# Kernel tuning notes

Measured on AMD Instinct MI355X. Metric: run time of the kernel, lower is better.

## Reference

```python
import jax, jax.numpy as jnp
import numpy as np

WS = 14          # window size
NH = 12          # num heads
C = 768          # hidden dim
HD = C // NH     # head dim = 64
MLP = 3072       # mlp dim
EPS = 1e-6


def _layernorm(x, g, b):
    mu = jnp.mean(x, axis=-1, keepdims=True)
    var = jnp.mean(jnp.square(x - mu), axis=-1, keepdims=True)
    return (x - mu) * jax.lax.rsqrt(var + EPS) * g + b


def setup_inputs() -> dict:
    key = jax.random.key(0)
    ks = jax.random.split(key, 8)
    B, H, W = 8, 64, 64
    f32 = jnp.float32
    d = {}
    d["x"] = jax.random.normal(ks[0], (B, H, W, C), f32)
    d["ln1_g"] = jnp.ones((C,), f32)
    d["ln1_b"] = jnp.zeros((C,), f32)
    d["qkv_w"] = (jax.random.normal(ks[1], (C, 3 * C), f32) * 0.02)
    d["qkv_b"] = jnp.zeros((3 * C,), f32)
    d["proj_w"] = (jax.random.normal(ks[2], (C, C), f32) * 0.02)
    d["proj_b"] = jnp.zeros((C,), f32)
    d["rel_pos_h"] = (jax.random.normal(ks[3], (2 * WS - 1, HD), f32) * 0.02)
    d["rel_pos_w"] = (jax.random.normal(ks[4], (2 * WS - 1, HD), f32) * 0.02)
    d["ln2_g"] = jnp.ones((C,), f32)
    d["ln2_b"] = jnp.zeros((C,), f32)
    d["mlp_w1"] = (jax.random.normal(ks[5], (C, MLP), f32) * 0.02)
    d["mlp_b1"] = jnp.zeros((MLP,), f32)
    d["mlp_w2"] = (jax.random.normal(ks[6], (MLP, C), f32) * 0.02)
    d["mlp_b2"] = jnp.zeros((C,), f32)
    return d


def reference(x, ln1_g, ln1_b, qkv_w, qkv_b, proj_w, proj_b,
              rel_pos_h, rel_pos_w, ln2_g, ln2_b,
              mlp_w1, mlp_b1, mlp_w2, mlp_b2):
    B, H, W, _ = x.shape
    xn = _layernorm(x, ln1_g, ln1_b)

    # ---- window partition (pad to multiple of WS) ----
    pad_h = (-H) % WS
    pad_w = (-W) % WS
    Hp, Wp = H + pad_h, W + pad_w
    xp = jnp.pad(xn, ((0, 0), (0, pad_h), (0, pad_w), (0, 0)))
    # [B, Hp/WS, WS, Wp/WS, WS, C] -> [Bn, WS, WS, C]
    win = xp.reshape(B, Hp // WS, WS, Wp // WS, WS, C)
    win = win.transpose(0, 1, 3, 2, 4, 5).reshape(-1, WS, WS, C)
    Bn = win.shape[0]
    N = WS * WS

    # ---- attention with decomposed relative position bias ----
    qkv = win.reshape(Bn, N, C) @ qkv_w + qkv_b                 # [Bn, N, 3C]
    qkv = qkv.reshape(Bn, N, 3, NH, HD).transpose(2, 0, 3, 1, 4)
    qkv = qkv.reshape(3, Bn * NH, N, HD)
    q, k, v = qkv[0], qkv[1], qkv[2]

    scale = HD ** -0.5
    attn = jnp.einsum('bnd,bmd->bnm', q * scale, k)             # [Bn*NH, N, N]

    # rel coords: q_size == k_size == WS, rel_pos already has 2*WS-1 rows
    coords = jnp.arange(WS)[:, None] - jnp.arange(WS)[None, :] + (WS - 1)
    Rh = rel_pos_h[coords]                                      # [WS, WS, HD]
    Rw = rel_pos_w[coords]                                      # [WS, WS, HD]
    rq = q.reshape(Bn * NH, WS, WS, HD)
    rel_h = jnp.einsum('bhwc,hkc->bhwk', rq, Rh)                # [B', WS, WS, WS]
    rel_w = jnp.einsum('bhwc,wkc->bhwk', rq, Rw)
    attn = (attn.reshape(Bn * NH, WS, WS, WS, WS)
            + rel_h[:, :, :, :, None]
            + rel_w[:, :, :, None, :]).reshape(Bn * NH, N, N)

    attn = jax.nn.softmax(attn, axis=-1)
    out = jnp.einsum('bnm,bmd->bnd', attn, v)                   # [Bn*NH, N, HD]
    out = out.reshape(Bn, NH, WS, WS, HD).transpose(0, 2, 3, 1, 4).reshape(Bn, WS, WS, C)
    out = out @ proj_w + proj_b

    # ---- window unpartition ----
    out = out.reshape(B, Hp // WS, Wp // WS, WS, WS, C)
    out = out.transpose(0, 1, 3, 2, 4, 5).reshape(B, Hp, Wp, C)[:, :H, :W, :]

    x1 = x + out
    y = _layernorm(x1, ln2_g, ln2_b)
    y = jax.nn.gelu(y @ mlp_w1 + mlp_b1, approximate=False) @ mlp_w2 + mlp_b2
    return x1 + y
```

## Files before the change

kernel.cpp:

```cpp
#include <hip/hip_runtime.h>
#include <hip/hip_bf16.h>
#include <cstdint>
#include <cstddef>

using bf16 = __hip_bfloat16;
typedef __attribute__((ext_vector_type(8))) short short8;
typedef __attribute__((ext_vector_type(4))) float f32x4;

typedef __attribute__((address_space(1))) const void as1_void;
typedef __attribute__((address_space(3))) void as3_void;

__device__ __forceinline__ f32x4 mfma16x16x32(short8 a, short8 b, f32x4 c) {
  return __builtin_amdgcn_mfma_f32_16x16x32_bf16(a, b, c, 0, 0, 0);
}

__device__ __forceinline__ void gload_lds16(const void* g, void* l) {
  __builtin_amdgcn_global_load_lds((as1_void*)g, (as3_void*)l, 16, 0, 0);
}

__device__ __forceinline__ uint32_t cvtpk(float a, float b) {
  uint32_t r;
  asm("v_cvt_pk_bf16_f32 %0, %1, %2" : "=v"(r) : "v"(a), "v"(b));
  return r;
}


static constexpr int MROWS = 39200;
static constexpr int MPAD  = 39296;
static constexpr int TOK2  = 32768;

__global__ __launch_bounds__(256)
void transpose_cast(const float* __restrict__ in, bf16* __restrict__ out, int K, int N) {
  __shared__ float t[32][33];
  const int tx = threadIdx.x & 31, ty = threadIdx.x >> 5;
  const int bx = blockIdx.x, by = blockIdx.y;
  const int x = bx * 32 + tx;
  for (int r = ty; r < 32; r += 8)
    t[r][tx] = in[(size_t)(by * 32 + r) * N + x];
  __syncthreads();
  const int xo = by * 32 + tx;
  for (int r = ty; r < 32; r += 8)
    out[(size_t)(bx * 32 + r) * K + xo] = __float2bfloat16(t[tx][r]);
}

__global__ __launch_bounds__(256)
void ln1_partition(const float* __restrict__ x, const float* __restrict__ g,
                   const float* __restrict__ bb, bf16* __restrict__ out) {
  const int token = blockIdx.x * 4 + (threadIdx.x >> 6);
  const int lane = threadIdx.x & 63;
  const int win = token / 196, tok = token % 196;
  const int b_ = win / 25, wh = (win / 5) % 5, ww = win % 5;
  const int i = tok / 14, j = tok % 14;
  const int h = wh * 14 + i, w = ww * 14 + j;
  bf16* o = out + (size_t)token * 768;
  if (h >= 64 || w >= 64) {
    for (int t = 0; t < 12; ++t) o[lane + 64 * t] = __float2bfloat16(0.f);
    return;
  }
  const float* src = x + ((size_t)((b_ * 64 + h) * 64 + w)) * 768;
  float vals[12], s = 0.f, ss = 0.f;
  #pragma unroll
  for (int t = 0; t < 12; ++t) {
    float v = src[lane + 64 * t];
    vals[t] = v; s += v; ss += v * v;
  }
  #pragma unroll
  for (int d = 32; d > 0; d >>= 1) { s += __shfl_xor(s, d); ss += __shfl_xor(ss, d); }
  const float mu = s * (1.f / 768.f);
  const float var = ss * (1.f / 768.f) - mu * mu;
  const float inv = rsqrtf(var + 1e-6f);
  #pragma unroll
  for (int t = 0; t < 12; ++t) {
    const int c = lane + 64 * t;
    o[c] = __float2bfloat16((vals[t] - mu) * inv * g[c] + bb[c]);
  }
}

__global__ __launch_bounds__(256)
void ln2_kernel(const float* __restrict__ x1, const float* __restrict__ g,
                const float* __restrict__ bb, bf16* __restrict__ out) {
  const int token = blockIdx.x * 4 + (threadIdx.x >> 6);
  const int lane = threadIdx.x & 63;
  const float* src = x1 + (size_t)token * 768;
  bf16* o = out + (size_t)token * 768;
  float vals[12], s = 0.f, ss = 0.f;
  #pragma unroll
  for (int t = 0; t < 12; ++t) {
    float v = src[lane + 64 * t];
    vals[t] = v; s += v; ss += v * v;
  }
  #pragma unroll
  for (int d = 32; d > 0; d >>= 1) { s += __shfl_xor(s, d); ss += __shfl_xor(ss, d); }
  const float mu = s * (1.f / 768.f);
  const float var = ss * (1.f / 768.f) - mu * mu;
  const float inv = rsqrtf(var + 1e-6f);
  #pragma unroll
  for (int t = 0; t < 12; ++t) {
    const int c = lane + 64 * t;
    o[c] = __float2bfloat16((vals[t] - mu) * inv * g[c] + bb[c]);
  }
}

template<int EPI>
__global__ __launch_bounds__(256)
void gemm_bf16(const bf16* __restrict__ A, const bf16* __restrict__ Bt,
               const float* __restrict__ bias, int K, int Mreal,
               const float* __restrict__ fin, float* __restrict__ fout,
               bf16* __restrict__ ob0, bf16* __restrict__ ob1, bf16* __restrict__ ob2) {
  __shared__ __align__(16) bf16 SMEM[16384];
  bf16* const lA[2] = { SMEM, SMEM + 4096 };
  bf16* const lB[2] = { SMEM + 8192, SMEM + 12288 };
  const int tid = threadIdx.x;
  const int lane = tid & 63, wv = tid >> 6;
  const int lr = lane & 15, hi = lane >> 4;
  const int wm = wv >> 1, wn = wv & 1;

  const int gx = gridDim.x;
  const int nwg = gx * gridDim.y;
  int lin = blockIdx.y * gx + blockIdx.x;
  {
    const int q8 = nwg >> 3, r8 = nwg & 7;
    const int xcd = lin & 7, pos = lin >> 3;
    lin = (xcd < r8 ? xcd * (q8 + 1) : r8 * (q8 + 1) + (xcd - r8) * q8) + pos;
  }
  const size_t arow0 = (size_t)(lin / gx) * 128;
  const size_t brow0 = (size_t)(lin % gx) * 128;
  f32x4 acc[4][4] = {};

  auto stage = [&](bf16* bufA, bf16* bufB, int kt) {
    const int k0 = kt * 32;
    #pragma unroll
    for (int it = 0; it < 2; ++it) {
      const int seg = it * 256 + tid;
      const int row = seg >> 2, kq = seg & 3;
      const size_t dst = (size_t)(it * 256 + wv * 64) * 8;
      if constexpr (EPI == 1) {
        const int k = k0 + kq * 8;
        gload_lds16(A + ((size_t)(k >> 6) * MPAD + arow0 + row) * 64 + (k & 63), bufA + dst);
      } else {
        gload_lds16(A + (arow0 + row) * K + k0 + kq * 8, bufA + dst);
      }
      gload_lds16(Bt + (brow0 + row) * K + k0 + kq * 8, bufB + dst);
    }
  };
  auto compute = [&](const bf16* bufA, const bf16* bufB) {
    short8 af[4], bfr[4];
    #pragma unroll
    for (int m = 0; m < 4; ++m) af[m] = *(const short8*)&bufA[(wm * 64 + m * 16 + lr) * 32 + hi * 8];
    #pragma unroll
    for (int n = 0; n < 4; ++n) bfr[n] = *(const short8*)&bufB[(wn * 64 + n * 16 + lr) * 32 + hi * 8];
    #pragma unroll
    for (int m = 0; m < 4; ++m)
      #pragma unroll
      for (int n = 0; n < 4; ++n)
        acc[m][n] = mfma16x16x32(af[m], bfr[n], acc[m][n]);
  };

  const int nt = K >> 5;
  stage(lA[0], lB[0], 0);
  __syncthreads();
  for (int t = 0; t < nt; t += 2) {
    if (t + 1 < nt) stage(lA[1], lB[1], t + 1);
    compute(lA[0], lB[0]);
    __syncthreads();
    if (t + 2 < nt) stage(lA[0], lB[0], t + 2);
    compute(lA[1], lB[1]);
    __syncthreads();
  }

  if constexpr (EPI == 0 || EPI == 2) {
    bf16* ct = SMEM;
    #pragma unroll
    for (int n = 0; n < 4; ++n) {
      const int col = wn * 64 + n * 16 + lr;
      const float bv = bias[(int)brow0 + col];
      #pragma unroll
      for (int m = 0; m < 4; ++m) {
        #pragma unroll
        for (int e = 0; e < 4; ++e) {
          const int row = wm * 64 + m * 16 + hi * 4 + e;
          float v = acc[m][n][e] + bv;
          if constexpr (EPI == 2) v = 0.5f * v * (1.f + erff(v * 0.70710678118f));
          const int byte = (row << 8) + (col << 1);
          *(bf16*)((char*)ct + (byte ^ ((row & 7) << 5))) = __float2bfloat16(v);
        }
      }
    }
    __syncthreads();
    #pragma unroll
    for (int i = 0; i < 8; ++i) {
      const int lin16 = i * 256 + tid;
      const int row = lin16 >> 4;
      const int u   = lin16 & 15;
      const int byte = (row << 8) + (u << 4);
      const short8 val = *(const short8*)((char*)ct + (byte ^ ((row & 7) << 5)));
      const int grow = (int)arow0 + row;
      const int gcol = (int)brow0 + u * 8;
      if constexpr (EPI == 0) {
        if (grow < Mreal) {
          const int which = gcol / 768, head = (gcol >> 6) % 12, d = gcol & 63;
          bf16* dstb = (which == 0) ? ob0 : ((which == 1) ? ob1 : ob2);
          *(short8*)&dstb[((size_t)head * MPAD + grow) * 64 + d] = val;
        }
      } else {
        *(short8*)&ob0[(size_t)grow * 3072 + gcol] = val;
      }
    }
  } else {
    #pragma unroll
    for (int n = 0; n < 4; ++n) {
      const int col = (int)brow0 + wn * 64 + n * 16 + lr;
      const float bv = bias[col];
      #pragma unroll
      for (int m = 0; m < 4; ++m) {
        #pragma unroll
        for (int e = 0; e < 4; ++e) {
          const int row = (int)arow0 + wm * 64 + m * 16 + hi * 4 + e;
          const float v = acc[m][n][e] + bv;
          if constexpr (EPI == 1) {
            if (row < Mreal) {
              const int win = row / 196, tok = row % 196;
              const int b_ = win / 25, wh = (win / 5) % 5, ww = win % 5;
              const int i = tok / 14, j = tok % 14;
              const int h = wh * 14 + i, w = ww * 14 + j;
              if (h < 64 && w < 64) {
                const size_t idx = ((size_t)((b_ * 64 + h) * 64 + w)) * 768 + col;
                fout[idx] = fin[idx] + v;
              }
            }
          } else {
            const size_t idx = (size_t)row * 768 + col;
            fout[idx] = fin[idx] + v;
          }
        }
      }
    }
  }
}

__global__ __launch_bounds__(256)
void attn_kernel(const bf16* __restrict__ qb, const bf16* __restrict__ kb,
                 const bf16* __restrict__ vb, const float* __restrict__ rph,
                 const float* __restrict__ rpw, bf16* __restrict__ aout) {
  __shared__ __align__(16) char SM[65248];
  bf16* pbh    = (bf16*)SM;
  bf16* pbw    = (bf16*)(SM + 4096);
  bf16* Gh     = (bf16*)(SM + 8192);
  bf16* Gw     = (bf16*)(SM + 23168);
  char* klds   = SM;
  char* vtb    = SM + 25600;
  bf16* relh_s = (bf16*)(SM + 54272);
  bf16* relw_s = (bf16*)(SM + 59760);

  const int bh = blockIdx.x;
  const int win = bh / 12, head = bh % 12;
  const size_t base = ((size_t)head * MPAD + win * 196) * 64;
  const bf16* Q  = qb + base;
  const bf16* Kp = kb + base;
  const bf16* Vp = vb + base;
  const int tid = threadIdx.x, lane = tid & 63, wv = tid >> 6;
  const int lr = lane & 15, hi = lane >> 4;

  for (int i = tid; i < 32 * 64; i += 256) {
    const int r = i >> 6, c = i & 63;
    const bool ok = r < 27;
    pbh[i] = __float2bfloat16(ok ? rph[r * 64 + c] : 0.f);
    pbw[i] = __float2bfloat16(ok ? rpw[r * 64 + c] : 0.f);
  }
  __syncthreads();
  {
    short8 bh00 = *(const short8*)&pbh[(lr) * 64 + hi * 8];
    short8 bh01 = *(const short8*)&pbh[(lr) * 64 + 32 + hi * 8];
    short8 bh10 = *(const short8*)&pbh[(16 + lr) * 64 + hi * 8];
    short8 bh11 = *(const short8*)&pbh[(16 + lr) * 64 + 32 + hi * 8];
    short8 bw00 = *(const short8*)&pbw[(lr) * 64 + hi * 8];
    short8 bw01 = *(const short8*)&pbw[(lr) * 64 + 32 + hi * 8];
    short8 bw10 = *(const short8*)&pbw[(16 + lr) * 64 + hi * 8];
    short8 bw11 = *(const short8*)&pbw[(16 + lr) * 64 + 32 + hi * 8];
    for (int mt = wv; mt < 13; mt += 4) {
      const short8 a0 = *(const short8*)&Q[(mt * 16 + lr) * 64 + hi * 8];
      const short8 a1 = *(const short8*)&Q[(mt * 16 + lr) * 64 + 32 + hi * 8];
      f32x4 g0 = {}, g1 = {}, g2 = {}, g3 = {};
      g0 = mfma16x16x32(a0, bh00, g0); g0 = mfma16x16x32(a1, bh01, g0);
      g1 = mfma16x16x32(a0, bh10, g1); g1 = mfma16x16x32(a1, bh11, g1);
      g2 = mfma16x16x32(a0, bw00, g2); g2 = mfma16x16x32(a1, bw01, g2);
      g3 = mfma16x16x32(a0, bw10, g3); g3 = mfma16x16x32(a1, bw11, g3);
      #pragma unroll
      for (int e = 0; e < 4; ++e) {
        const int row = mt * 16 + hi * 4 + e;
        Gh[row * 36 + lr]      = __float2bfloat16(g0[e]);
        Gh[row * 36 + 16 + lr] = __float2bfloat16(g1[e]);
        Gw[row * 36 + lr]      = __float2bfloat16(g2[e]);
        Gw[row * 36 + 16 + lr] = __float2bfloat16(g3[e]);
      }
    }
  }
  __syncthreads();
  bf16 ghr[11], gwr[11];
  #pragma unroll
  for (int t = 0; t < 11; ++t) {
    const int i = tid + t * 256;
    if (i < 196 * 14) {
      const int q = i / 14, kk = i - (i / 14) * 14;
      const int rh = q / 14 - kk + 13;
      const int rw2 = q - (q / 14) * 14 - kk + 13;
      ghr[t] = Gh[q * 36 + rh];
      gwr[t] = Gw[q * 36 + rw2];
    }
  }
  __syncthreads();
  #pragma unroll
  for (int t = 0; t < 11; ++t) {
    const int i = tid + t * 256;
    if (i < 196 * 14) { relh_s[i] = ghr[t]; relw_s[i] = gwr[t]; }
  }
  for (int c = wv; c < 25; c += 4) {
    const int row = c * 8 + (lane >> 3);
    const int ch  = (lane & 7) ^ (row & 7);
    gload_lds16(Kp + row * 64 + ch * 8, klds + c * 1024);
  }
  for (int i = tid; i < 196 * 8; i += 256) {
    const int key = i >> 3, dg = (i & 7) * 8;
    const short8 v = *(const short8*)&Vp[key * 64 + dg];
    #pragma unroll
    for (int j = 0; j < 8; ++j) {
      const int idx = (dg + j) * 448 + key * 2;
      *(bf16*)(vtb + (idx ^ (j << 4))) = ((const bf16*)&v)[j];
    }
  }
  for (int i = tid; i < 64 * 28; i += 256) {
    const int d = i / 28, key = 196 + i - (i / 28) * 28;
    const int idx = d * 448 + key * 2;
    *(bf16*)(vtb + (idx ^ ((d & 7) << 4))) = __float2bfloat16(0.f);
  }
  __syncthreads();

  for (int qt = wv; qt < 13; qt += 4) {
    const int q = qt * 16 + lr;
    const int qc = q < 196 ? q : 195;
    const short8 bq0 = *(const short8*)&Q[(qt * 16 + lr) * 64 + hi * 8];
    const short8 bq1 = *(const short8*)&Q[(qt * 16 + lr) * 64 + 32 + hi * 8];
    f32x4 s[13];
    __builtin_amdgcn_s_setprio(1);
    #pragma unroll
    for (int nt = 0; nt < 13; ++nt) {
      const int key = nt * 16 + lr;
      const char* kr = klds + key * 128;
      const short8 ka0 = *(const short8*)(kr + (((hi) ^ (key & 7)) << 4));
      const short8 ka1 = *(const short8*)(kr + (((hi + 4) ^ (key & 7)) << 4));
      f32x4 z = {};
      z = mfma16x16x32(ka0, bq0, z);
      z = mfma16x16x32(ka1, bq1, z);
      s[nt] = z;
    }
    __builtin_amdgcn_s_setprio(0);
    float mx = -3.0e38f;
    #pragma unroll
    for (int nt = 0; nt < 13; ++nt) {
      #pragma unroll
      for (int e = 0; e < 4; ++e) {
        const int key = nt * 16 + hi * 4 + e;
        const int kh = key / 14, kw = key - kh * 14;
        float v = s[nt][e] * 0.125f + __bfloat162float(relh_s[qc * 14 + kh])
                                    + __bfloat162float(relw_s[qc * 14 + kw]);
        v = (key < 196) ? v : -3.0e38f;
        s[nt][e] = v;
        mx = fmaxf(mx, v);
      }
    }
    mx = fmaxf(mx, __shfl_xor(mx, 16));
    mx = fmaxf(mx, __shfl_xor(mx, 32));
    float sm = 0.f;
    #pragma unroll
    for (int nt = 0; nt < 13; ++nt)
      #pragma unroll
      for (int e = 0; e < 4; ++e) {
        const float p = __expf(s[nt][e] - mx);
        s[nt][e] = p; sm += p;
      }
    sm += __shfl_xor(sm, 16);
    sm += __shfl_xor(sm, 32);
    const float rinv = 1.f / sm;
    f32x4 o[4] = {};
    #pragma unroll
    for (int kk = 0; kk < 7; ++kk) {
      const uint32_t x0 = cvtpk(s[2 * kk][0] * rinv, s[2 * kk][1] * rinv);
      const uint32_t x1 = cvtpk(s[2 * kk][2] * rinv, s[2 * kk][3] * rinv);
      const uint32_t y0 = cvtpk(s[2 * kk + 1][0] * rinv, s[2 * kk + 1][1] * rinv);
      const uint32_t y1 = cvtpk(s[2 * kk + 1][2] * rinv, s[2 * kk + 1][3] * rinv);
      const uint32_t s0 = (hi < 2) ? y0 : x0, s1 = (hi < 2) ? y1 : x1;
      const uint32_t t0 = __shfl_xor(s0, 32), t1 = __shfl_xor(s1, 32);
      const uint32_t o0 = (hi < 2) ? x0 : y0, o1 = (hi < 2) ? x1 : y1;
      const bool sendOwn = (hi == 1) || (hi == 2);
      const uint32_t u0 = sendOwn ? o0 : t0, u1 = sendOwn ? o1 : t1;
      const uint32_t r0 = __shfl_xor(u0, 16), r1 = __shfl_xor(u1, 16);
      union { uint32_t u[4]; short8 v; } pf;
      pf.u[0] = (hi == 0) ? x0 : ((hi == 2) ? t0 : r0);
      pf.u[1] = (hi == 0) ? x1 : ((hi == 2) ? t1 : r1);
      pf.u[2] = (hi == 3) ? y0 : ((hi == 1) ? t0 : r0);
      pf.u[3] = (hi == 3) ? y1 : ((hi == 1) ? t1 : r1);
      __builtin_amdgcn_s_setprio(1);
      #pragma unroll
      for (int n2 = 0; n2 < 4; ++n2) {
        const int d = n2 * 16 + lr;
        const int idx = d * 448 + (kk * 32 + hi * 8) * 2;
        const short8 va = *(const short8*)(vtb + (idx ^ ((lr & 7) << 4)));
        o[n2] = mfma16x16x32(va, pf.v, o[n2]);
      }
      __builtin_amdgcn_s_setprio(0);
    }
    if (q < 196) {
      bf16* orow = aout + ((size_t)head * MPAD + win * 196 + q) * 64;
      #pragma unroll
      for (int n2 = 0; n2 < 4; ++n2) {
        uint32_t d0 = cvtpk(o[n2][0], o[n2][1]);
        uint32_t d1 = cvtpk(o[n2][2], o[n2][3]);
        uint32_t* dst = (uint32_t*)&orow[n2 * 16 + hi * 4];
        dst[0] = d0; dst[1] = d1;
      }
    }
  }
}

extern "C" void kernel_launch(void* const* d_in, const int* in_sizes, int n_in,
                              void* d_out, int out_size, void* d_ws, size_t ws_size,
                              hipStream_t stream) {
  (void)in_sizes; (void)n_in; (void)out_size; (void)ws_size;
  const float* x      = (const float*)d_in[0];
  const float* ln1_g  = (const float*)d_in[1];
  const float* ln1_b  = (const float*)d_in[2];
  const float* qkv_w  = (const float*)d_in[3];
  const float* qkv_b  = (const float*)d_in[4];
  const float* proj_w = (const float*)d_in[5];
  const float* proj_b = (const float*)d_in[6];
  const float* rph    = (const float*)d_in[7];
  const float* rpw    = (const float*)d_in[8];
  const float* ln2_g  = (const float*)d_in[9];
  const float* ln2_b  = (const float*)d_in[10];
  const float* w1     = (const float*)d_in[11];
  const float* b1v    = (const float*)d_in[12];
  const float* w2     = (const float*)d_in[13];
  const float* b2v    = (const float*)d_in[14];
  float* outp = (float*)d_out;

  char* ws = (char*)d_ws;
  size_t off = 0;
  auto alloc = [&](size_t bytes) { char* p = ws + off; off += (bytes + 255) & ~(size_t)255; return p; };
  bf16* qkv_wt  = (bf16*)alloc((size_t)2304 * 768 * 2);
  bf16* proj_wt = (bf16*)alloc((size_t)768 * 768 * 2);
  bf16* w1t     = (bf16*)alloc((size_t)3072 * 768 * 2);
  bf16* w2t     = (bf16*)alloc((size_t)768 * 3072 * 2);
  const size_t szB1 = (size_t)MPAD * 768 * 2;
  const size_t szB2 = (size_t)TOK2 * 768 * 2;
  char* regB = alloc(szB1 > szB2 ? szB1 : szB2);
  const size_t szQKV = (size_t)3 * 12 * MPAD * 64 * 2;
  const size_t szH   = (size_t)TOK2 * 3072 * 2;
  char* regC = alloc(szQKV > szH ? szQKV : szH);

  bf16* xnwin   = (bf16*)regB;
  bf16* attnout = (bf16*)regB;
  bf16* xn2     = (bf16*)regB;
  bf16* qbuf    = (bf16*)regC;
  bf16* kbuf    = qbuf + (size_t)12 * MPAD * 64;
  bf16* vbuf    = kbuf + (size_t)12 * MPAD * 64;
  bf16* hbuf    = (bf16*)regC;

  transpose_cast<<<dim3(2304 / 32, 768 / 32), 256, 0, stream>>>(qkv_w, qkv_wt, 768, 2304);
  transpose_cast<<<dim3(768 / 32, 768 / 32), 256, 0, stream>>>(proj_w, proj_wt, 768, 768);
  transpose_cast<<<dim3(3072 / 32, 768 / 32), 256, 0, stream>>>(w1, w1t, 768, 3072);
  transpose_cast<<<dim3(768 / 32, 3072 / 32), 256, 0, stream>>>(w2, w2t, 3072, 768);

  ln1_partition<<<dim3(MROWS / 4), 256, 0, stream>>>(x, ln1_g, ln1_b, xnwin);

  gemm_bf16<0><<<dim3(2304 / 128, MPAD / 128), 256, 0, stream>>>(
      xnwin, qkv_wt, qkv_b, 768, MROWS, nullptr, nullptr, qbuf, kbuf, vbuf);

  attn_kernel<<<dim3(2400), 256, 0, stream>>>(qbuf, kbuf, vbuf, rph, rpw, attnout);

  gemm_bf16<1><<<dim3(768 / 128, MPAD / 128), 256, 0, stream>>>(
      attnout, proj_wt, proj_b, 768, MROWS, x, outp, nullptr, nullptr, nullptr);

  ln2_kernel<<<dim3(TOK2 / 4), 256, 0, stream>>>(outp, ln2_g, ln2_b, xn2);

  gemm_bf16<2><<<dim3(3072 / 128, TOK2 / 128), 256, 0, stream>>>(
      xn2, w1t, b1v, 768, TOK2, nullptr, nullptr, hbuf, nullptr, nullptr);
  gemm_bf16<3><<<dim3(768 / 128, TOK2 / 128), 256, 0, stream>>>(
      hbuf, w2t, b2v, 3072, TOK2, outp, outp, nullptr, nullptr, nullptr);
}
```

Before: 1.135 ms.

## Deepen GEMM load pipeline with explicit vmcnt waits and use tanh GELU

The GEMM main loop now preloads two K-tiles and uses explicit s_waitcnt vmcnt plus raw s_barrier and sched_barrier instead of __syncthreads. This lets the next tile's global-to-LDS loads stay in flight while the current tile is computed. The MLP epilogue also swaps exact erf GELU for a tanh approximation built on __expf. That is cheaper but departs numerically from the reference's exact GELU, and the hand-tuned vmcnt(4) count must match the number of loads each stage issues.

```diff
diff --git a/kernel.cpp b/kernel.cpp
--- a/kernel.cpp
+++ b/kernel.cpp
@@ -24,6 +24,15 @@
   return r;
 }
 
+__device__ __forceinline__ void vmwait4() { asm volatile("s_waitcnt vmcnt(4)" ::: "memory"); }
+__device__ __forceinline__ void vmwait0() { asm volatile("s_waitcnt vmcnt(0)" ::: "memory"); }
+
+__device__ __forceinline__ float gelu_f(float v) {
+  const float u = 0.7978845608f * v * (1.f + 0.044715f * v * v);
+  const float e = __expf(-2.f * fabsf(u));
+  const float t = (1.f - e) / (1.f + e);
+  return 0.5f * v * (1.f + (u < 0.f ? -t : t));
+}
 
 static constexpr int MROWS = 39200;
 static constexpr int MPAD  = 39296;
@@ -108,8 +117,10 @@
                const float* __restrict__ fin, float* __restrict__ fout,
                bf16* __restrict__ ob0, bf16* __restrict__ ob1, bf16* __restrict__ ob2) {
   __shared__ __align__(16) bf16 SMEM[16384];
-  bf16* const lA[2] = { SMEM, SMEM + 4096 };
-  bf16* const lB[2] = { SMEM + 8192, SMEM + 12288 };
+  bf16* const lA0 = SMEM;
+  bf16* const lA1 = SMEM + 4096;
+  bf16* const lB0 = SMEM + 8192;
+  bf16* const lB1 = SMEM + 12288;
   const int tid = threadIdx.x;
   const int lane = tid & 63, wv = tid >> 6;
   const int lr = lane & 15, hi = lane >> 4;
@@ -157,15 +168,23 @@
   };
 
   const int nt = K >> 5;
-  stage(lA[0], lB[0], 0);
-  __syncthreads();
+  stage(lA0, lB0, 0);
+  stage(lA1, lB1, 1);
   for (int t = 0; t < nt; t += 2) {
-    if (t + 1 < nt) stage(lA[1], lB[1], t + 1);
-    compute(lA[0], lB[0]);
-    __syncthreads();
-    if (t + 2 < nt) stage(lA[0], lB[0], t + 2);
-    compute(lA[1], lB[1]);
-    __syncthreads();
+    vmwait4();
+    __builtin_amdgcn_s_barrier();
+    __builtin_amdgcn_sched_barrier(0);
+    compute(lA0, lB0);
+    __builtin_amdgcn_sched_barrier(0);
+    __builtin_amdgcn_s_barrier();
+    if (t + 2 < nt) { stage(lA0, lB0, t + 2); vmwait4(); }
+    else            { vmwait0(); }
+    __builtin_amdgcn_s_barrier();
+    __builtin_amdgcn_sched_barrier(0);
+    compute(lA1, lB1);
+    __builtin_amdgcn_sched_barrier(0);
+    __builtin_amdgcn_s_barrier();
+    if (t + 3 < nt) stage(lA1, lB1, t + 3);
   }
 
   if constexpr (EPI == 0 || EPI == 2) {
@@ -180,7 +199,7 @@
         for (int e = 0; e < 4; ++e) {
           const int row = wm * 64 + m * 16 + hi * 4 + e;
           float v = acc[m][n][e] + bv;
-          if constexpr (EPI == 2) v = 0.5f * v * (1.f + erff(v * 0.70710678118f));
+          if constexpr (EPI == 2) v = gelu_f(v);
           const int byte = (row << 8) + (col << 1);
           *(bf16*)((char*)ct + (byte ^ ((row & 7) << 5))) = __float2bfloat16(v);
         }
```

Measured after the change: 1.140 ms. About the same (+0.5%).
